# Kernel tuning notes

Hardware: AMD Instinct MI355X
Metric: run time of the kernel (lower is better)

Reference implementation:

```python
import jax, jax.numpy as jnp
import numpy as np

N = 100000
E = 1000000
N_FEAT = 128
N_HID = 16
N_HEAD = 8
HIDDEN = N_HID * N_HEAD  # 128
N_CLASS = 64
NEG_SLOPE = 0.2


def layer_norm(x, g, b, eps=1e-5):
    mu = x.mean(-1, keepdims=True)
    var = ((x - mu) ** 2).mean(-1, keepdims=True)
    return (x - mu) * jax.lax.rsqrt(var + eps) * g + b


def gat_conv(x, src, dst, W, a_src, a_dst, bias, concat):
    # Standard GATConv math (PyG): project, per-head additive attention,
    # softmax over incoming edges (self-loops included), weighted scatter-sum.
    H, C = a_src.shape
    n = x.shape[0]
    h = (x @ W).reshape(n, H, C)                      # [N,H,C]
    al = jnp.einsum('nhc,hc->nh', h, a_src)           # [N,H]
    ar = jnp.einsum('nhc,hc->nh', h, a_dst)
    e = jax.nn.leaky_relu(al[src] + ar[dst], NEG_SLOPE)  # [E',H]
    m = jax.ops.segment_max(e, dst, num_segments=n)
    m = jnp.where(jnp.isfinite(m), m, 0.0)
    ee = jnp.exp(e - m[dst])
    den = jax.ops.segment_sum(ee, dst, num_segments=n)
    alpha = ee / (den[dst] + 1e-16)                   # [E',H]
    out = jax.ops.segment_sum(h[src] * alpha[:, :, None], dst, num_segments=n)
    out = out.reshape(n, H * C) if concat else out.mean(1)
    return out + bias, h, alpha


def setup_inputs() -> dict:
    key = jax.random.key(0)
    ks = jax.random.split(key, 20)
    s = lambda *sh: 1.0 / np.sqrt(sh[-1])
    inp = {
        'x': jax.random.normal(ks[0], (N, N_FEAT), jnp.float32),
        'edge_index': jax.random.randint(ks[1], (2, E), 0, N, jnp.int32),
        # layer 1: n_feat -> n_hid x n_head (concat)
        'W1': jax.random.normal(ks[2], (N_FEAT, HIDDEN), jnp.float32) * s(N_FEAT),
        'a_src1': jax.random.normal(ks[3], (N_HEAD, N_HID), jnp.float32) * s(N_HID),
        'a_dst1': jax.random.normal(ks[4], (N_HEAD, N_HID), jnp.float32) * s(N_HID),
        'b1': jnp.zeros((HIDDEN,), jnp.float32),
        'g1': jnp.ones((HIDDEN,), jnp.float32),
        'be1': jnp.zeros((HIDDEN,), jnp.float32),
        # layer 2: hidden -> hidden (concat)
        'W2': jax.random.normal(ks[5], (HIDDEN, HIDDEN), jnp.float32) * s(HIDDEN),
        'a_src2': jax.random.normal(ks[6], (N_HEAD, N_HID), jnp.float32) * s(N_HID),
        'a_dst2': jax.random.normal(ks[7], (N_HEAD, N_HID), jnp.float32) * s(N_HID),
        'b2': jnp.zeros((HIDDEN,), jnp.float32),
        'g2': jnp.ones((HIDDEN,), jnp.float32),
        'be2': jnp.zeros((HIDDEN,), jnp.float32),
        # out layer: hidden -> n_class, 1 head, concat=False
        'W3': jax.random.normal(ks[8], (HIDDEN, N_CLASS), jnp.float32) * s(HIDDEN),
        'a_src3': jax.random.normal(ks[9], (1, N_CLASS), jnp.float32) * s(N_CLASS),
        'a_dst3': jax.random.normal(ks[10], (1, N_CLASS), jnp.float32) * s(N_CLASS),
        'b3': jnp.zeros((N_CLASS,), jnp.float32),
        'g3': jnp.ones((N_CLASS,), jnp.float32),
        'be3': jnp.zeros((N_CLASS,), jnp.float32),
    }
    return inp


def reference(x, edge_index, W1, a_src1, a_dst1, b1, g1, be1,
              W2, a_src2, a_dst2, b2, g2, be2,
              W3, a_src3, a_dst3, b3, g3, be3):
    # add self loops (GATConv default)
    loops = jnp.arange(N, dtype=edge_index.dtype)
    src = jnp.concatenate([edge_index[0], loops])
    dst = jnp.concatenate([edge_index[1], loops])
    # Transductive path, eval mode (dropout is identity)
    x, _, _ = gat_conv(x, src, dst, W1, a_src1, a_dst1, b1, concat=True)
    x = jax.nn.elu(layer_norm(x, g1, be1))
    x, _, _ = gat_conv(x, src, dst, W2, a_src2, a_dst2, b2, concat=True)
    x = jax.nn.elu(layer_norm(x, g2, be2))
    x, _, _ = gat_conv(x, src, dst, W3, a_src3, a_dst3, b3, concat=False)
    x = layer_norm(x, g3, be3)
    return x
```

## Files before the change

kernel.cpp:

```cpp
#include <hip/hip_runtime.h>
#include <math.h>

#define N_NODES 100000
#define N_EDGES 1000000
#define EP_EDGES (N_EDGES + N_NODES)
#define NBKT ((N_NODES + 255) / 256)
#define PAD 48

typedef short bf16x8 __attribute__((ext_vector_type(8)));
typedef float f32x4 __attribute__((ext_vector_type(4)));


__device__ inline unsigned bf16pack(float a, float b) {
    unsigned ua = __float_as_uint(a);
    unsigned ub = __float_as_uint(b);
    ua += 0x7FFFu + ((ua >> 16) & 1u);
    ub += 0x7FFFu + ((ub >> 16) & 1u);
    return (ua >> 16) | (ub & 0xFFFF0000u);
}

__device__ inline unsigned short bf16r(float a) {
    unsigned u = __float_as_uint(a);
    u += 0x7FFFu + ((u >> 16) & 1u);
    return (unsigned short)(u >> 16);
}

__device__ inline int swz(int o) { return o ^ (((o >> 8) & 7) << 4); }


__global__ void bkt_count(const int* __restrict__ ei, int* __restrict__ bktCnt) {
    __shared__ int hist[NBKT];
    int tid = threadIdx.x;
    for (int j = tid; j < NBKT; j += 256) hist[j] = 0;
    __syncthreads();
    int e0 = blockIdx.x * 4096;
    int e1 = min(e0 + 4096, EP_EDGES);
    for (int e = e0 + tid; e < e1; e += 256) {
        int d = (e < N_EDGES) ? ei[N_EDGES + e] : (e - N_EDGES);
        atomicAdd(&hist[d >> 8], 1);
    }
    __syncthreads();
    for (int j = tid; j < NBKT; j += 256) {
        int c = hist[j];
        if (c) atomicAdd(&bktCnt[j], c);
    }
}

__global__ void bkt_scan(const int* __restrict__ bktCnt, int* __restrict__ bktBase,
                         int* __restrict__ bktCursor) {
    __shared__ int tmp[512];
    int tid = threadIdx.x;
    int v = (tid < NBKT) ? bktCnt[tid] : 0;
    tmp[tid] = v;
    __syncthreads();
    int run = v;
    for (int off = 1; off < 512; off <<= 1) {
        int add = (tid >= off) ? tmp[tid - off] : 0;
        __syncthreads();
        run += add;
        tmp[tid] = run;
        __syncthreads();
    }
    if (tid <= NBKT) {
        int base = run - v;
        bktBase[tid] = base;
        if (tid < NBKT) bktCursor[tid] = base;
    }
}

__global__ void bkt_scatter(const int* __restrict__ ei, int* __restrict__ bktCursor,
                            unsigned* __restrict__ bktEdges) {
    __shared__ int hist[NBKT], chunk[NBKT];
    int tid = threadIdx.x;
    for (int j = tid; j < NBKT; j += 256) hist[j] = 0;
    __syncthreads();
    int e0 = blockIdx.x * 2048;
    int e1 = min(e0 + 2048, EP_EDGES);
    for (int e = e0 + tid; e < e1; e += 256) {
        int d = (e < N_EDGES) ? ei[N_EDGES + e] : (e - N_EDGES);
        atomicAdd(&hist[d >> 8], 1);
    }
    __syncthreads();
    for (int j = tid; j < NBKT; j += 256) {
        int c = hist[j];
        chunk[j] = c ? atomicAdd(&bktCursor[j], c) : 0;
        hist[j] = 0;
    }
    __syncthreads();
    for (int e = e0 + tid; e < e1; e += 256) {
        int s, d;
        if (e < N_EDGES) { s = ei[e]; d = ei[N_EDGES + e]; }
        else             { s = d = e - N_EDGES; }
        int b = d >> 8;
        int off = atomicAdd(&hist[b], 1);
        bktEdges[chunk[b] + off] = (unsigned)s | ((unsigned)(d & 255) << 24);
    }
}

__global__ void bkt_final(const unsigned* __restrict__ bktEdges, const int* __restrict__ bktBase,
                          int* __restrict__ deg_arr, int* __restrict__ pad_src) {
    __shared__ int hist[256], cur[256];
    int tid = threadIdx.x;
    int b = blockIdx.x;
    int base = bktBase[b], end = bktBase[b + 1];
    hist[tid] = 0;
    cur[tid] = 0;
    __syncthreads();
    for (int i = base + tid; i < end; i += 256)
        atomicAdd(&hist[bktEdges[i] >> 24], 1);
    __syncthreads();
    int node = b * 256 + tid;
    if (node < N_NODES) deg_arr[node] = min(hist[tid], PAD);
    __syncthreads();
    for (int i = base + tid; i < end; i += 256) {
        unsigned u = bktEdges[i];
        int d = u >> 24;
        int pos = atomicAdd(&cur[d], 1);
        if (pos < PAD)
            pad_src[(size_t)(b * 256 + d) * PAD + pos] = (int)(u & 0xFFFFFFu);
    }
    __syncthreads();
    for (int idx = tid; idx < 256 * PAD; idx += 256) {
        int dloc = idx / PAD, j = idx % PAD;
        int nd = b * 256 + dloc;
        if (nd < N_NODES && j >= min(hist[dloc], PAD))
            pad_src[(size_t)nd * PAD + j] = nd;
    }
}


template <int COUT>
__global__ void wt_prep(const float* __restrict__ W, unsigned short* __restrict__ Wt) {
    int t = blockIdx.x * 256 + threadIdx.x;
    if (t >= 128 * COUT) return;
    int k = t / COUT, c = t % COUT;
    Wt[c * 128 + k] = bf16r(W[t]);
}


template <int COUT, int H, bool IN_F32>
__launch_bounds__(256)
__global__ void gemm_mfma(const void* __restrict__ Xv, const unsigned short* __restrict__ Wt,
                          const float* __restrict__ a_src, const float* __restrict__ a_dst,
                          unsigned* __restrict__ hb16, float* __restrict__ al,
                          float* __restrict__ ar, int n) {
    constexpr int NT = COUT / 16;
    __shared__ unsigned char lds[16384 + COUT * 256 + 1024];
    unsigned char* sx = lds;
    unsigned char* sw = lds + 16384;
    float* sc = (float*)sw;

    int tid = threadIdx.x;
    int row0 = blockIdx.x * 64;
    int lane = tid & 63;
    int wv = tid >> 6;

    if (IN_F32) {
        const float* Xf = (const float*)Xv;
        for (int c = tid; c < 1024; c += 256) {
            int o = c * 16;
            int row = o >> 8;
            int k0 = (o & 255) >> 1;
            int gr = row0 + row;
            float4 f0 = make_float4(0.f, 0.f, 0.f, 0.f), f1 = f0;
            if (gr < n) {
                f0 = *(const float4*)(Xf + (size_t)gr * 128 + k0);
                f1 = *(const float4*)(Xf + (size_t)gr * 128 + k0 + 4);
            }
            *(uint4*)(sx + swz(o)) = make_uint4(bf16pack(f0.x, f0.y), bf16pack(f0.z, f0.w),
                                                bf16pack(f1.x, f1.y), bf16pack(f1.z, f1.w));
        }
    } else {
        const unsigned char* Xb = (const unsigned char*)Xv;
        for (int c = tid; c < 1024; c += 256) {
            int o = c * 16;
            int row = o >> 8;
            int gr = row0 + row;
            uint4 v = make_uint4(0u, 0u, 0u, 0u);
            if (gr < n) v = *(const uint4*)(Xb + (size_t)gr * 256 + (o & 255));
            *(uint4*)(sx + swz(o)) = v;
        }
    }
    for (int c = tid; c < COUT * 16; c += 256) {
        int o = c * 16;
        *(uint4*)(sw + swz(o)) = *(const uint4*)((const unsigned char*)Wt + o);
    }
    __syncthreads();

    f32x4 acc[NT];
#pragma unroll
    for (int t = 0; t < NT; ++t) acc[t] = (f32x4){0.f, 0.f, 0.f, 0.f};
    int arow = wv * 16 + (lane & 15);
    int kg = lane >> 4;
#pragma unroll
    for (int s = 0; s < 4; ++s) {
        int ko = s * 64 + kg * 16;
        bf16x8 a = *(const bf16x8*)(sx + swz(arow * 256 + ko));
#pragma unroll
        for (int t = 0; t < NT; ++t) {
            bf16x8 bfr = *(const bf16x8*)(sw + swz((t * 16 + (lane & 15)) * 256 + ko));
            acc[t] = __builtin_amdgcn_mfma_f32_16x16x32_bf16(a, bfr, acc[t], 0, 0, 0);
        }
    }
    __syncthreads();

#pragma unroll
    for (int t = 0; t < NT; ++t)
#pragma unroll
        for (int i = 0; i < 4; ++i)
            sc[(wv * 16 + kg * 4 + i) * (COUT + 4) + t * 16 + (lane & 15)] = acc[t][i];
    __syncthreads();

    constexpr int NCG = COUT / 8;
    constexpr int ROWS = 64 * NCG / 256;
    int tc = tid % NCG, tr = tid / NCG;
    float asv[8], adv[8];
#pragma unroll
    for (int j = 0; j < 8; ++j) {
        asv[j] = a_src[tc * 8 + j];
        adv[j] = a_dst[tc * 8 + j];
    }
#pragma unroll
    for (int i = 0; i < ROWS; ++i) {
        int row = tr * ROWS + i;
        int gr = row0 + row;
        float h8[8];
        *(float4*)&h8[0] = *(const float4*)(sc + row * (COUT + 4) + tc * 8);
        *(float4*)&h8[4] = *(const float4*)(sc + row * (COUT + 4) + tc * 8 + 4);
        float pa = 0.f, pb = 0.f;
#pragma unroll
        for (int j = 0; j < 8; ++j) {
            pa = fmaf(h8[j], asv[j], pa);
            pb = fmaf(h8[j], adv[j], pb);
        }
        if (COUT / H == 16) {
            pa += __shfl_xor(pa, 1);
            pb += __shfl_xor(pb, 1);
            if ((tc & 1) == 0 && gr < n) {
                al[gr * H + (tc >> 1)] = pa;
                ar[gr * H + (tc >> 1)] = pb;
            }
        } else {
            pa += __shfl_xor(pa, 1); pb += __shfl_xor(pb, 1);
            pa += __shfl_xor(pa, 2); pb += __shfl_xor(pb, 2);
            pa += __shfl_xor(pa, 4); pb += __shfl_xor(pb, 4);
            if (tc == 0 && gr < n) {
                al[gr] = pa;
                ar[gr] = pb;
            }
        }
        if (gr < n) {
            *(uint4*)(hb16 + (size_t)gr * (COUT / 2) + tc * 4) =
                make_uint4(bf16pack(h8[0], h8[1]), bf16pack(h8[2], h8[3]),
                           bf16pack(h8[4], h8[5]), bf16pack(h8[6], h8[7]));
        }
    }
}


template <int H, int COUT, bool DO_ELU, bool OUTBF>
__launch_bounds__(256)
__global__ void gat_fused(const unsigned* __restrict__ hb16, const float* __restrict__ al,
                          const float* __restrict__ ar, const int* __restrict__ deg_arr,
                          const int* __restrict__ pad_src, const float* __restrict__ bias,
                          const float* __restrict__ gamma, const float* __restrict__ beta,
                          void* __restrict__ outx, int n) {
    constexpr bool PAIR = (COUT == 128);
    int node = blockIdx.x * 4 + (threadIdx.x >> 6);
    node = __builtin_amdgcn_readfirstlane(node);
    int l = threadIdx.x & 63;
    if (node >= n) return;

    int deg = deg_arr[node];
    const int* sp = pad_src + (size_t)node * PAD;
    const unsigned short* hbs = (const unsigned short*)hb16;

    float acc0 = 0.f, acc1 = 0.f, den;
    int c0 = PAIR ? 2 * l : l;

    if (PAIR) {
        int eh = l & 7;
        int ej = l >> 3;
        int hc = l >> 3;
        float ar_e = ar[node * 8 + eh];
        float den_p;

        int s_lo = sp[ej];
        float a_lo = al[s_lo * 8 + eh];
        unsigned rv_lo[8];
#pragma unroll
        for (int j = 0; j < 8; ++j) {
            int sj = __builtin_amdgcn_readlane(s_lo, j * 8);
            rv_lo[j] = hb16[(size_t)sj * 64 + l];
        }
        float e0 = a_lo + ar_e; e0 = (e0 >= 0.f) ? e0 : 0.2f * e0;
        float w_lo = (ej < deg) ? __expf(e0) : 0.f;
        den_p = w_lo;

        if (deg > 8) {
            int s_hi = sp[8 + ej];
            float a_hi = al[s_hi * 8 + eh];
            unsigned rv_hi[8];
#pragma unroll
            for (int j = 0; j < 8; ++j) {
                int sj = __builtin_amdgcn_readlane(s_hi, j * 8);
                rv_hi[j] = hb16[(size_t)sj * 64 + l];
            }
            float e1 = a_hi + ar_e; e1 = (e1 >= 0.f) ? e1 : 0.2f * e1;
            float w_hi = (8 + ej < deg) ? __expf(e1) : 0.f;
            den_p += w_hi;
#pragma unroll
            for (int j = 0; j < 8; ++j) {
                float wj = __shfl(w_hi, j * 8 + hc);
                acc0 = fmaf(wj, __uint_as_float(rv_hi[j] << 16), acc0);
                acc1 = fmaf(wj, __uint_as_float(rv_hi[j] & 0xFFFF0000u), acc1);
            }
        }
#pragma unroll
        for (int j = 0; j < 8; ++j) {
            float wj = __shfl(w_lo, j * 8 + hc);
            acc0 = fmaf(wj, __uint_as_float(rv_lo[j] << 16), acc0);
            acc1 = fmaf(wj, __uint_as_float(rv_lo[j] & 0xFFFF0000u), acc1);
        }
        for (int k = 16; k < deg; k += 8) {
            int s_c = sp[k + ej];
            float a = al[s_c * 8 + eh];
            float e = a + ar_e; e = (e >= 0.f) ? e : 0.2f * e;
            float w = (k + ej < deg) ? __expf(e) : 0.f;
            den_p += w;
            unsigned rv[8];
#pragma unroll
            for (int j = 0; j < 8; ++j) {
                int sj = __builtin_amdgcn_readlane(s_c, j * 8);
                rv[j] = hb16[(size_t)sj * 64 + l];
            }
#pragma unroll
            for (int j = 0; j < 8; ++j) {
                float wj = __shfl(w, j * 8 + hc);
                acc0 = fmaf(wj, __uint_as_float(rv[j] << 16), acc0);
                acc1 = fmaf(wj, __uint_as_float(rv[j] & 0xFFFF0000u), acc1);
            }
        }
        for (int off = 8; off < 64; off <<= 1) den_p += __shfl_xor(den_p, off);
        den = __shfl(den_p, hc);
    } else {
        float ar_e = ar[node];
        int idx = l < PAD ? l : PAD - 1;
        int s_cur = sp[idx];
        float a = al[s_cur];
        float e = a + ar_e; e = (e >= 0.f) ? e : 0.2f * e;
        float w = (l < deg) ? __expf(e) : 0.f;
        float den_p = w;
        int nsub = (deg + 7) >> 3;
        for (int sub = 0; sub < nsub; ++sub) {
            unsigned short rv[8];
#pragma unroll
            for (int j2 = 0; j2 < 8; ++j2) {
                int sj = __builtin_amdgcn_readlane(s_cur, sub * 8 + j2);
                rv[j2] = hbs[(size_t)sj * 64 + l];
            }
#pragma unroll
            for (int j2 = 0; j2 < 8; ++j2) {
                float wj = __uint_as_float(
                    __builtin_amdgcn_readlane(__float_as_uint(w), sub * 8 + j2));
                acc0 = fmaf(wj, __uint_as_float(((unsigned)rv[j2]) << 16), acc0);
            }
        }
        for (int off = 1; off < 64; off <<= 1) den_p += __shfl_xor(den_p, off);
        den = den_p;
    }

    float inv = 1.f / (den + 1e-16f);
    float v0 = acc0 * inv + bias[c0];
    float v1 = 0.f;
    float ssum = v0;
    if (PAIR) { v1 = acc1 * inv + bias[c0 + 1]; ssum += v1; }
    for (int off = 1; off < 64; off <<= 1) ssum += __shfl_xor(ssum, off);
    float mean = ssum / COUT;
    float d0 = v0 - mean, d1 = v1 - mean;
    float vs = PAIR ? (d0 * d0 + d1 * d1) : d0 * d0;
    for (int off = 1; off < 64; off <<= 1) vs += __shfl_xor(vs, off);
    float rstd = rsqrtf(vs / COUT + 1e-5f);
    float y0 = d0 * rstd * gamma[c0] + beta[c0];
    if (DO_ELU) y0 = (y0 > 0.f) ? y0 : expm1f(y0);
    if (PAIR) {
        float y1 = d1 * rstd * gamma[c0 + 1] + beta[c0 + 1];
        if (DO_ELU) y1 = (y1 > 0.f) ? y1 : expm1f(y1);
        if (OUTBF) {
            ((unsigned*)outx)[(size_t)node * 64 + l] = bf16pack(y0, y1);
        } else {
            *(float2*)((float*)outx + (size_t)node * COUT + c0) = make_float2(y0, y1);
        }
    } else {
        ((float*)outx)[(size_t)node * COUT + c0] = y0;
    }
}


extern "C" void kernel_launch(void* const* d_in, const int* in_sizes, int n_in,
                              void* d_out, int out_size, void* d_ws, size_t ws_size,
                              hipStream_t stream) {
    const float* x   = (const float*)d_in[0];
    const int*   ei  = (const int*)d_in[1];
    const float* W1  = (const float*)d_in[2];
    const float* as1 = (const float*)d_in[3];
    const float* ad1 = (const float*)d_in[4];
    const float* b1  = (const float*)d_in[5];
    const float* g1  = (const float*)d_in[6];
    const float* be1 = (const float*)d_in[7];
    const float* W2  = (const float*)d_in[8];
    const float* as2 = (const float*)d_in[9];
    const float* ad2 = (const float*)d_in[10];
    const float* b2  = (const float*)d_in[11];
    const float* g2  = (const float*)d_in[12];
    const float* be2 = (const float*)d_in[13];
    const float* W3  = (const float*)d_in[14];
    const float* as3 = (const float*)d_in[15];
    const float* ad3 = (const float*)d_in[16];
    const float* b3  = (const float*)d_in[17];
    const float* g3  = (const float*)d_in[18];
    const float* be3 = (const float*)d_in[19];
    float* out = (float*)d_out;

    char* p = (char*)d_ws;
    auto alloc = [&](size_t bytes) -> char* {
        char* r = p;
        p += (bytes + 255) & ~size_t(255);
        return r;
    };
    unsigned* hb16   = (unsigned*)alloc((size_t)N_NODES * 64 * 4);
    unsigned* xbuf   = (unsigned*)alloc((size_t)N_NODES * 64 * 4);
    float* al        = (float*)alloc((size_t)N_NODES * 8 * 4);
    float* ar        = (float*)alloc((size_t)N_NODES * 8 * 4);
    int*   deg_arr   = (int*)alloc((size_t)N_NODES * 4);
    int*   pad_src   = (int*)alloc((size_t)N_NODES * PAD * 4);
    unsigned* bktEdges = (unsigned*)alloc((size_t)EP_EDGES * 4);
    int*   bktCnt    = (int*)alloc((size_t)(NBKT + 1) * 4);
    int*   bktBase   = (int*)alloc((size_t)(NBKT + 1) * 4);
    int*   bktCursor = (int*)alloc((size_t)(NBKT + 1) * 4);
    unsigned short* Wt1 = (unsigned short*)alloc((size_t)128 * 128 * 2);
    unsigned short* Wt2 = (unsigned short*)alloc((size_t)128 * 128 * 2);
    unsigned short* Wt3 = (unsigned short*)alloc((size_t)64 * 128 * 2);

    hipMemsetAsync(bktCnt, 0, (size_t)(NBKT + 1) * 4, stream);

    wt_prep<128><<<64, 256, 0, stream>>>(W1, Wt1);
    wt_prep<128><<<64, 256, 0, stream>>>(W2, Wt2);
    wt_prep<64><<<32, 256, 0, stream>>>(W3, Wt3);

    bkt_count<<<(EP_EDGES + 4095) / 4096, 256, 0, stream>>>(ei, bktCnt);
    bkt_scan<<<1, 512, 0, stream>>>(bktCnt, bktBase, bktCursor);
    bkt_scatter<<<(EP_EDGES + 2047) / 2048, 256, 0, stream>>>(ei, bktCursor, bktEdges);
    bkt_final<<<NBKT, 256, 0, stream>>>(bktEdges, bktBase, deg_arr, pad_src);

    const int gemm_grid = (N_NODES + 63) / 64;
    const int agg_grid  = (N_NODES + 3) / 4;

    gemm_mfma<128, 8, true><<<gemm_grid, 256, 0, stream>>>(x, Wt1, as1, ad1,
                                                           hb16, al, ar, N_NODES);
    gat_fused<8, 128, true, true><<<agg_grid, 256, 0, stream>>>(hb16, al, ar, deg_arr, pad_src,
                                                                b1, g1, be1, xbuf, N_NODES);
    gemm_mfma<128, 8, false><<<gemm_grid, 256, 0, stream>>>(xbuf, Wt2, as2, ad2,
                                                            hb16, al, ar, N_NODES);
    gat_fused<8, 128, true, true><<<agg_grid, 256, 0, stream>>>(hb16, al, ar, deg_arr, pad_src,
                                                                b2, g2, be2, xbuf, N_NODES);
    gemm_mfma<64, 1, false><<<gemm_grid, 256, 0, stream>>>(xbuf, Wt3, as3, ad3,
                                                           hb16, al, ar, N_NODES);
    gat_fused<1, 64, false, false><<<agg_grid, 256, 0, stream>>>(hb16, al, ar, deg_arr, pad_src,
                                                                 b3, g3, be3, out, N_NODES);
}
```

Before: 282.3 us.

## Store source attention logits in bf16, fold denominators, merge weight prep kernels

Source attention logits are stored as bf16 instead of fp32, which halves the bytes of the per-edge random gathers in aggregation. The first 16 edges' weights are exchanged through LDS rather than shuffles, and the softmax denominator is accumulated per lane from the broadcast weights, removing the separate cross-lane reduction. The three weight-transpose kernels are merged into one launch, bias/gamma/beta loads are hoisted, and expm1f is replaced by __expf-1. The risks are lower precision in the attention logits and in ELU near zero, plus extra LDS traffic.

```diff
diff --git a/kernel.cpp b/kernel.cpp
--- a/kernel.cpp
+++ b/kernel.cpp
@@ -23,6 +23,10 @@
     unsigned u = __float_as_uint(a);
     u += 0x7FFFu + ((u >> 16) & 1u);
     return (unsigned short)(u >> 16);
+}
+
+__device__ inline float bf16f(unsigned short v) {
+    return __uint_as_float(((unsigned)v) << 16);
 }
 
 __device__ inline int swz(int o) { return o ^ (((o >> 8) & 7) << 4); }
@@ -129,12 +133,20 @@
 }
 
 
-template <int COUT>
-__global__ void wt_prep(const float* __restrict__ W, unsigned short* __restrict__ Wt) {
+__global__ void wt_prep_all(const float* __restrict__ W1, const float* __restrict__ W2,
+                            const float* __restrict__ W3, unsigned short* __restrict__ Wt1,
+                            unsigned short* __restrict__ Wt2, unsigned short* __restrict__ Wt3) {
     int t = blockIdx.x * 256 + threadIdx.x;
-    if (t >= 128 * COUT) return;
-    int k = t / COUT, c = t % COUT;
-    Wt[c * 128 + k] = bf16r(W[t]);
+    if (t < 128 * 128) {
+        int k = t >> 7, c = t & 127;
+        Wt1[c * 128 + k] = bf16r(W1[t]);
+        Wt2[c * 128 + k] = bf16r(W2[t]);
+    }
+    int t3 = t - 128 * 128;
+    if (t3 >= 0 && t3 < 128 * 64) {
+        int k = t3 >> 6, c = t3 & 63;
+        Wt3[c * 128 + k] = bf16r(W3[t3]);
+    }
 }
 
 
@@ -142,7 +154,7 @@
 __launch_bounds__(256)
 __global__ void gemm_mfma(const void* __restrict__ Xv, const unsigned short* __restrict__ Wt,
                           const float* __restrict__ a_src, const float* __restrict__ a_dst,
-                          unsigned* __restrict__ hb16, float* __restrict__ al,
+                          unsigned* __restrict__ hb16, unsigned short* __restrict__ alb,
                           float* __restrict__ ar, int n) {
     constexpr int NT = COUT / 16;
     __shared__ unsigned char lds[16384 + COUT * 256 + 1024];
@@ -237,7 +249,7 @@
             pa += __shfl_xor(pa, 1);
             pb += __shfl_xor(pb, 1);
             if ((tc & 1) == 0 && gr < n) {
-                al[gr * H + (tc >> 1)] = pa;
+                alb[gr * H + (tc >> 1)] = bf16r(pa);
                 ar[gr * H + (tc >> 1)] = pb;
             }
         } else {
@@ -245,7 +257,7 @@
             pa += __shfl_xor(pa, 2); pb += __shfl_xor(pb, 2);
             pa += __shfl_xor(pa, 4); pb += __shfl_xor(pb, 4);
             if (tc == 0 && gr < n) {
-                al[gr] = pa;
+                alb[gr] = bf16r(pa);
                 ar[gr] = pb;
             }
         }
@@ -260,33 +272,39 @@
 
 template <int H, int COUT, bool DO_ELU, bool OUTBF>
 __launch_bounds__(256)
-__global__ void gat_fused(const unsigned* __restrict__ hb16, const float* __restrict__ al,
+__global__ void gat_fused(const unsigned* __restrict__ hb16, const unsigned short* __restrict__ alb,
                           const float* __restrict__ ar, const int* __restrict__ deg_arr,
                           const int* __restrict__ pad_src, const float* __restrict__ bias,
                           const float* __restrict__ gamma, const float* __restrict__ beta,
                           void* __restrict__ outx, int n) {
     constexpr bool PAIR = (COUT == 128);
+    __shared__ float wbuf[4][128];
     int node = blockIdx.x * 4 + (threadIdx.x >> 6);
     node = __builtin_amdgcn_readfirstlane(node);
     int l = threadIdx.x & 63;
+    int wv = threadIdx.x >> 6;
     if (node >= n) return;
 
     int deg = deg_arr[node];
     const int* sp = pad_src + (size_t)node * PAD;
     const unsigned short* hbs = (const unsigned short*)hb16;
 
-    float acc0 = 0.f, acc1 = 0.f, den;
     int c0 = PAIR ? 2 * l : l;
+    float bias0 = bias[c0], gam0 = gamma[c0], bet0 = beta[c0];
+    float bias1 = 0.f, gam1 = 0.f, bet1 = 0.f;
+    if (PAIR) { bias1 = bias[c0 + 1]; gam1 = gamma[c0 + 1]; bet1 = beta[c0 + 1]; }
+
+    float acc0 = 0.f, acc1 = 0.f, den = 0.f;
 
     if (PAIR) {
         int eh = l & 7;
         int ej = l >> 3;
         int hc = l >> 3;
         float ar_e = ar[node * 8 + eh];
-        float den_p;
+        bool hi = deg > 8;
 
         int s_lo = sp[ej];
-        float a_lo = al[s_lo * 8 + eh];
+        float a_lo = bf16f(alb[s_lo * 8 + eh]);
         unsigned rv_lo[8];
 #pragma unroll
         for (int j = 0; j < 8; ++j) {
@@ -295,39 +313,38 @@
         }
         float e0 = a_lo + ar_e; e0 = (e0 >= 0.f) ? e0 : 0.2f * e0;
         float w_lo = (ej < deg) ? __expf(e0) : 0.f;
-        den_p = w_lo;
-
-        if (deg > 8) {
+        float w_hi = 0.f;
+        unsigned rv_hi[8];
+        if (hi) {
             int s_hi = sp[8 + ej];
-            float a_hi = al[s_hi * 8 + eh];
-            unsigned rv_hi[8];
+            float a_hi = bf16f(alb[s_hi * 8 + eh]);
 #pragma unroll
             for (int j = 0; j < 8; ++j) {
                 int sj = __builtin_amdgcn_readlane(s_hi, j * 8);
                 rv_hi[j] = hb16[(size_t)sj * 64 + l];
             }
             float e1 = a_hi + ar_e; e1 = (e1 >= 0.f) ? e1 : 0.2f * e1;
-            float w_hi = (8 + ej < deg) ? __expf(e1) : 0.f;
-            den_p += w_hi;
-#pragma unroll
-            for (int j = 0; j < 8; ++j) {
-                float wj = __shfl(w_hi, j * 8 + hc);
-                acc0 = fmaf(wj, __uint_as_float(rv_hi[j] << 16), acc0);
-                acc1 = fmaf(wj, __uint_as_float(rv_hi[j] & 0xFFFF0000u), acc1);
-            }
-        }
+            w_hi = (8 + ej < deg) ? __expf(e1) : 0.f;
+        }
+
+        *(float2*)&wbuf[wv][2 * l] = make_float2(w_lo, w_hi);
 #pragma unroll
         for (int j = 0; j < 8; ++j) {
-            float wj = __shfl(w_lo, j * 8 + hc);
-            acc0 = fmaf(wj, __uint_as_float(rv_lo[j] << 16), acc0);
-            acc1 = fmaf(wj, __uint_as_float(rv_lo[j] & 0xFFFF0000u), acc1);
-        }
+            float2 wj = *(const float2*)&wbuf[wv][2 * (j * 8 + hc)];
+            den += wj.x + wj.y;
+            acc0 = fmaf(wj.x, __uint_as_float(rv_lo[j] << 16), acc0);
+            acc1 = fmaf(wj.x, __uint_as_float(rv_lo[j] & 0xFFFF0000u), acc1);
+            if (hi) {
+                acc0 = fmaf(wj.y, __uint_as_float(rv_hi[j] << 16), acc0);
+                acc1 = fmaf(wj.y, __uint_as_float(rv_hi[j] & 0xFFFF0000u), acc1);
+            }
+        }
+
         for (int k = 16; k < deg; k += 8) {
             int s_c = sp[k + ej];
-            float a = al[s_c * 8 + eh];
+            float a = bf16f(alb[s_c * 8 + eh]);
             float e = a + ar_e; e = (e >= 0.f) ? e : 0.2f * e;
             float w = (k + ej < deg) ? __expf(e) : 0.f;
-            den_p += w;
             unsigned rv[8];
 #pragma unroll
             for (int j = 0; j < 8; ++j) {
@@ -337,20 +354,18 @@
 #pragma unroll
             for (int j = 0; j < 8; ++j) {
                 float wj = __shfl(w, j * 8 + hc);
+                den += wj;
                 acc0 = fmaf(wj, __uint_as_float(rv[j] << 16), acc0);
                 acc1 = fmaf(wj, __uint_as_float(rv[j] & 0xFFFF0000u), acc1);
             }
         }
-        for (int off = 8; off < 64; off <<= 1) den_p += __shfl_xor(den_p, off);
-        den = __shfl(den_p, hc);
     } else {
         float ar_e = ar[node];
         int idx = l < PAD ? l : PAD - 1;
         int s_cur = sp[idx];
-        float a = al[s_cur];
+        float a = bf16f(alb[s_cur]);
         float e = a + ar_e; e = (e >= 0.f) ? e : 0.2f * e;
         float w = (l < deg) ? __expf(e) : 0.f;
-        float den_p = w;
         int nsub = (deg + 7) >> 3;
         for (int sub = 0; sub < nsub; ++sub) {
             unsigned short rv[8];
@@ -363,29 +378,28 @@
             for (int j2 = 0; j2 < 8; ++j2) {
                 float wj = __uint_as_float(
                     __builtin_amdgcn_readlane(__float_as_uint(w), sub * 8 + j2));
+                den += wj;
                 acc0 = fmaf(wj, __uint_as_float(((unsigned)rv[j2]) << 16), acc0);
             }
         }
-        for (int off = 1; off < 64; off <<= 1) den_p += __shfl_xor(den_p, off);
-        den = den_p;
     }
 
     float inv = 1.f / (den + 1e-16f);
-    float v0 = acc0 * inv + bias[c0];
+    float v0 = acc0 * inv + bias0;
     float v1 = 0.f;
     float ssum = v0;
-    if (PAIR) { v1 = acc1 * inv + bias[c0 + 1]; ssum += v1; }
+    if (PAIR) { v1 = acc1 * inv + bias1; ssum += v1; }
     for (int off = 1; off < 64; off <<= 1) ssum += __shfl_xor(ssum, off);
     float mean = ssum / COUT;
     float d0 = v0 - mean, d1 = v1 - mean;
     float vs = PAIR ? (d0 * d0 + d1 * d1) : d0 * d0;
     for (int off = 1; off < 64; off <<= 1) vs += __shfl_xor(vs, off);
     float rstd = rsqrtf(vs / COUT + 1e-5f);
-    float y0 = d0 * rstd * gamma[c0] + beta[c0];
-    if (DO_ELU) y0 = (y0 > 0.f) ? y0 : expm1f(y0);
+    float y0 = d0 * rstd * gam0 + bet0;
+    if (DO_ELU) y0 = (y0 > 0.f) ? y0 : (__expf(y0) - 1.f);
     if (PAIR) {
-        float y1 = d1 * rstd * gamma[c0 + 1] + beta[c0 + 1];
-        if (DO_ELU) y1 = (y1 > 0.f) ? y1 : expm1f(y1);
+        float y1 = d1 * rstd * gam1 + bet1;
+        if (DO_ELU) y1 = (y1 > 0.f) ? y1 : (__expf(y1) - 1.f);
         if (OUTBF) {
             ((unsigned*)outx)[(size_t)node * 64 + l] = bf16pack(y0, y1);
         } else {
@@ -430,7 +444,7 @@
     };
     unsigned* hb16   = (unsigned*)alloc((size_t)N_NODES * 64 * 4);
     unsigned* xbuf   = (unsigned*)alloc((size_t)N_NODES * 64 * 4);
-    float* al        = (float*)alloc((size_t)N_NODES * 8 * 4);
+    unsigned short* alb = (unsigned short*)alloc((size_t)N_NODES * 8 * 2);
     float* ar        = (float*)alloc((size_t)N_NODES * 8 * 4);
     int*   deg_arr   = (int*)alloc((size_t)N_NODES * 4);
     int*   pad_src   = (int*)alloc((size_t)N_NODES * PAD * 4);
@@ -444,9 +458,8 @@
 
     hipMemsetAsync(bktCnt, 0, (size_t)(NBKT + 1) * 4, stream);
 
-    wt_prep<128><<<64, 256, 0, stream>>>(W1, Wt1);
-    wt_prep<128><<<64, 256, 0, stream>>>(W2, Wt2);
-    wt_prep<64><<<32, 256, 0, stream>>>(W3, Wt3);
+    wt_prep_all<<<(128 * 128 + 128 * 64 + 255) / 256, 256, 0, stream>>>(W1, W2, W3,
+                                                                        Wt1, Wt2, Wt3);
 
     bkt_count<<<(EP_EDGES + 4095) / 4096, 256, 0, stream>>>(ei, bktCnt);
     bkt_scan<<<1, 512, 0, stream>>>(bktCnt, bktBase, bktCursor);
@@ -457,15 +470,15 @@
     const int agg_grid  = (N_NODES + 3) / 4;
 
     gemm_mfma<128, 8, true><<<gemm_grid, 256, 0, stream>>>(x, Wt1, as1, ad1,
-                                                           hb16, al, ar, N_NODES);
-    gat_fused<8, 128, true, true><<<agg_grid, 256, 0, stream>>>(hb16, al, ar, deg_arr, pad_src,
+                                                           hb16, alb, ar, N_NODES);
+    gat_fused<8, 128, true, true><<<agg_grid, 256, 0, stream>>>(hb16, alb, ar, deg_arr, pad_src,
                                                                 b1, g1, be1, xbuf, N_NODES);
     gemm_mfma<128, 8, false><<<gemm_grid, 256, 0, stream>>>(xbuf, Wt2, as2, ad2,
-                                                            hb16, al, ar, N_NODES);
-    gat_fused<8, 128, true, true><<<agg_grid, 256, 0, stream>>>(hb16, al, ar, deg_arr, pad_src,
+                                                            hb16, alb, ar, N_NODES);
+    gat_fused<8, 128, true, true><<<agg_grid, 256, 0, stream>>>(hb16, alb, ar, deg_arr, pad_src,
                                                                 b2, g2, be2, xbuf, N_NODES);
     gemm_mfma<64, 1, false><<<gemm_grid, 256, 0, stream>>>(xbuf, Wt3, as3, ad3,
-                                                           hb16, al, ar, N_NODES);
-    gat_fused<1, 64, false, false><<<agg_grid, 256, 0, stream>>>(hb16, al, ar, deg_arr, pad_src,
+                                                           hb16, alb, ar, N_NODES);
+    gat_fused<1, 64, false, false><<<agg_grid, 256, 0, stream>>>(hb16, alb, ar, deg_arr, pad_src,
                                                                  b3, g3, be3, out, N_NODES);
 }
```

New measurement: 262.7 us. -6.9%, faster.
